# Kernel tuning notes

Hardware: AMD Instinct MI355X
Metric: run time of the kernel (lower is better)

## Reference

```python
import jax, jax.numpy as jnp
import numpy as np

EPS = 1e-5
MOM = 0.9

def _ln(x, g, b):
    m = jnp.mean(x, axis=-1, keepdims=True)
    v = jnp.var(x, axis=-1, keepdims=True)
    return (x - m) / jnp.sqrt(v + EPS) * g + b

def _gelu(x):
    return jax.nn.gelu(x, approximate=False)  # torch default exact GELU


def setup_inputs() -> dict:
    S, B, d, K = 2048, 64, 256, 16
    key = jax.random.key(0)
    ks = jax.random.split(key, 12)
    def w(k, shape):
        return jax.random.normal(k, shape, dtype=jnp.float32) * 0.02
    return {
        'x': jax.random.normal(ks[0], (S, B, d), dtype=jnp.float32),
        'slot_init': w(ks[1], (K, d)),
        # Linear weights stored as (in, out): y = x @ W + b
        'Wq': w(ks[2], (d, d)), 'bq': jnp.zeros((d,), jnp.float32),
        'Wk': w(ks[3], (d, d)), 'bk': jnp.zeros((d,), jnp.float32),
        'Wv': w(ks[4], (d, d)), 'bv': jnp.zeros((d,), jnp.float32),
        'wg1_W': w(ks[5], (2 * d, d)), 'wg1_b': jnp.zeros((d,), jnp.float32),
        'wg2_W': w(ks[6], (d, 1)), 'wg2_b': jnp.zeros((1,), jnp.float32),
        'eg_W': w(ks[7], (2 * d, d)), 'eg_b': jnp.zeros((d,), jnp.float32),
        'wc_W': w(ks[8], (2 * d, d)), 'wc_b': jnp.zeros((d,), jnp.float32),
        'wc_ln_g': jnp.ones((d,), jnp.float32), 'wc_ln_b': jnp.zeros((d,), jnp.float32),
        'fu_W': w(ks[9], (2 * d, d)), 'fu_b': jnp.zeros((d,), jnp.float32),
        'fu_ln_g': jnp.ones((d,), jnp.float32), 'fu_ln_b': jnp.zeros((d,), jnp.float32),
        'on_g': jnp.ones((d,), jnp.float32), 'on_b': jnp.zeros((d,), jnp.float32),
    }


def reference(x, slot_init, Wq, bq, Wk, bk, Wv, bv, wg1_W, wg1_b, wg2_W, wg2_b,
              eg_W, eg_b, wc_W, wc_b, wc_ln_g, wc_ln_b, fu_W, fu_b,
              fu_ln_g, fu_ln_b, on_g, on_b):
    S, B, d = x.shape
    K = slot_init.shape[0]
    scale = d ** (-0.5)
    M0 = jnp.broadcast_to(slot_init[None], (B, K, d))            # [B,K,d]
    p0 = jnp.zeros((B, K), x.dtype)

    def step(carry, x_t):
        M, pers = carry
        q = x_t @ Wq + bq                                        # [B,d]
        k = M @ Wk + bk                                          # [B,K,d]
        v = M @ Wv + bv
        attn = jax.nn.softmax(jnp.einsum('bd,bkd->bk', q, k) * scale, axis=-1)
        r = jnp.einsum('bk,bkd->bd', attn, v)                    # [B,d]
        pers = MOM * pers + (1.0 - MOM) * attn
        cat = jnp.concatenate([x_t, r], axis=-1)                 # [B,2d]
        out_t = _ln(_gelu(cat @ fu_W + fu_b), fu_ln_g, fu_ln_b)  # dropout = eval/identity
        novelty = 1.0 - jnp.max(attn, axis=-1, keepdims=True)    # [B,1]
        g_w = jax.nn.sigmoid(_gelu(cat @ wg1_W + wg1_b) @ wg2_W + wg2_b) * novelty
        evict = jax.nn.softmax(-pers * 4.0, axis=-1)             # [B,K]
        sq = jnp.concatenate([jnp.broadcast_to(x_t[:, None], (B, K, d)), M], axis=-1)
        erase = jax.nn.sigmoid(sq @ eg_W + eg_b)                 # [B,K,d]
        write = _ln(_gelu(sq @ wc_W + wc_b), wc_ln_g, wc_ln_b)
        alpha = (g_w * evict)[..., None]                         # [B,K,1]
        M = M * (1.0 - alpha * erase) + alpha * write
        pers = pers + evict * g_w * 0.1
        return (M, pers), out_t

    (M, _), outs = jax.lax.scan(step, (M0, p0), x)
    x_aug = _ln(outs + x, on_g, on_b)                            # [S,B,d]
    proto = jnp.transpose(M, (1, 0, 2))                          # [K,B,d]
    return x_aug, proto
```

## Files before the change

### kernel.cpp

```cpp
#include <hip/hip_runtime.h>
#include <stdint.h>
#include <stddef.h>


#define SLEN 2048
#define NB   64
#define DD   256
#define KS   16
#define KVSTR 1026
#define TPB  512

typedef __attribute__((ext_vector_type(8))) short v8bf;
typedef __attribute__((ext_vector_type(4))) float v4f;

__device__ __forceinline__ float bf2f(uint16_t h){
  union { uint32_t u; float f; } v; v.u = ((uint32_t)h) << 16; return v.f;
}
__device__ __forceinline__ uint16_t f2bf(float f){
  union { float f; uint32_t u; } v; v.f = f;
  uint32_t u = v.u;
  return (uint16_t)((u + 0x7FFFu + ((u >> 16) & 1u)) >> 16);
}
__device__ __forceinline__ void splitf(float f, uint16_t& h, uint16_t& l){
  h = f2bf(f);
  l = f2bf(f - bf2f(h));
}
__device__ __forceinline__ float geluf(float xx){
  return 0.5f * xx * (1.0f + erff(xx * 0.70710678118654752f));
}
__device__ __forceinline__ float sigmf(float xx){
  return 1.0f / (1.0f + expf(-xx));
}
__device__ __forceinline__ v4f MFMA16(v8bf a, v8bf b, v4f c){
  return __builtin_amdgcn_mfma_f32_16x16x32_bf16(a, b, c, 0, 0, 0);
}

template<int RM>
__device__ __forceinline__ void ldA_f32(const char* base, int lane, int kc,
                                        v8bf& hi, v8bf& lo){
  int row = lane & RM;
  int off = row * 1024 + (((kc << 7) + ((lane >> 4) << 5)) ^ ((row & 7) << 5));
  const float* p = (const float*)(base + off);
  union { v8bf v; uint16_t u[8]; } H, L;
  #pragma unroll
  for (int j = 0; j < 8; ++j) splitf(p[j], H.u[j], L.u[j]);
  hi = H.v; lo = L.v;
}

__global__ __launch_bounds__(256) void prep_kernel(
    const float* __restrict__ Wq, const float* __restrict__ Wk, const float* __restrict__ Wv,
    const float* __restrict__ wg1W, const float* __restrict__ egW, const float* __restrict__ wcW,
    const float* __restrict__ fuW,
    const float* __restrict__ bq, const float* __restrict__ bwg1, const float* __restrict__ beg,
    const float* __restrict__ bwc, const float* __restrict__ bfu,
    const float* __restrict__ bk, const float* __restrict__ bv,
    uint16_t* __restrict__ wbigh, uint16_t* __restrict__ wbigl,
    uint16_t* __restrict__ wrfh,
    uint16_t* __restrict__ wxfh, uint16_t* __restrict__ wxfl,
    float* __restrict__ bxall, float* __restrict__ bkv)
{
  int idx = blockIdx.x * 256 + threadIdx.x;
  if (idx < 262144){
    int j = idx & 7, lane = (idx >> 3) & 63, kc = (idx >> 9) & 7, nt = idx >> 12;
    int k = kc*32 + ((lane >> 4) << 3) + j;
    int n = nt*16 + (lane & 15);
    float v;
    if (n < 256)      v = Wk[k*256 + n];
    else if (n < 512) v = Wv[k*256 + n - 256];
    else if (n < 768) v = egW[(256 + k)*256 + n - 512];
    else              v = wcW[(256 + k)*256 + n - 768];
    uint16_t h, l; splitf(v, h, l);
    wbigh[idx] = h; wbigl[idx] = l;
  }
  int i2 = idx - 262144;
  if (i2 >= 0 && i2 < 131072){
    int j = i2 & 7, lane = (i2 >> 3) & 63, kc = (i2 >> 9) & 7, nt = i2 >> 12;
    int k = kc*32 + ((lane >> 4) << 3) + j;
    int n = nt*16 + (lane & 15);
    float v = (n < 256) ? wg1W[(256 + k)*256 + n] : fuW[(256 + k)*256 + n - 256];
    wrfh[i2] = f2bf(v);
  }
  int i3 = idx - 393216;
  if (i3 >= 0 && i3 < 327680){
    int j = i3 & 7, lane = (i3 >> 3) & 63, kc = (i3 >> 9) & 7, nt = i3 >> 12;
    int k = kc*32 + ((lane >> 4) << 3) + j;
    int n = nt*16 + (lane & 15);
    float v;
    if (n < 256)       v = Wq[k*256 + n];
    else if (n < 512)  v = wg1W[k*256 + n - 256];
    else if (n < 768)  v = egW[k*256 + n - 512];
    else if (n < 1024) v = wcW[k*256 + n - 768];
    else               v = fuW[k*256 + n - 1024];
    uint16_t h, l; splitf(v, h, l);
    wxfh[i3] = h; wxfl[i3] = l;
  }
  int i4 = idx - 720896;
  if (i4 >= 0 && i4 < 1280){
    float v;
    if (i4 < 256)       v = bq[i4];
    else if (i4 < 512)  v = bwg1[i4 - 256];
    else if (i4 < 768)  v = beg[i4 - 512];
    else if (i4 < 1024) v = bwc[i4 - 768];
    else                v = bfu[i4 - 1024];
    bxall[i4] = v;
  }
  int i5 = idx - 722176;
  if (i5 >= 0 && i5 < 512){
    bkv[i5] = (i5 < 256) ? bk[i5] : bv[i5 - 256];
  }
}

#define SM_BYTES 134544

__global__ __launch_bounds__(TPB, 2) void memunit_kernel(
    const float* __restrict__ x, const float* __restrict__ slot_init,
    const float* __restrict__ wg2W, const float* __restrict__ wg2b,
    const float* __restrict__ wcg, const float* __restrict__ wcb,
    const float* __restrict__ fug, const float* __restrict__ fub,
    const float* __restrict__ ong, const float* __restrict__ onb,
    const uint16_t* __restrict__ wbigh, const uint16_t* __restrict__ wbigl,
    const uint16_t* __restrict__ wrfh,
    const uint16_t* __restrict__ wxfh, const uint16_t* __restrict__ wxfl,
    const float* __restrict__ bxall, const float* __restrict__ bkv,
    float* __restrict__ out)
{
  extern __shared__ char smem[];
  char*     MfB  = smem;
  char*     xbB  = smem + 16384;
  char*     rbB  = smem + 24576;
  float*    rb   = (float*)rbB;
  float*    kveg = (float*)(smem + 25600);
  float*    Xp   = (float*)(smem + 91264);
  float*    mv   = (float*)(smem + 132224);
  float*    sc   = (float*)(smem + 134272);

  const int b    = blockIdx.x;
  const int tid  = threadIdx.x;
  const int lane = tid & 63;
  const int wave = tid >> 6;
  const int grp  = tid & 31;

  const float wg2b0 = wg2b[0];

  auto mfp = [&](int s, int n) -> float* {
    return (float*)(MfB + s*1024 + (((n*4)) ^ ((s & 7) << 5)));
  };

  {
    int s = tid >> 5;
    int c0 = grp * 8;
    #pragma unroll
    for (int jj = 0; jj < 8; ++jj)
      *mfp(s, c0 + jj) = slot_init[s*256 + c0 + jj];
    if (tid < 256) rb[tid] = 0.0f;
    if (tid < 16)  sc[16 + tid] = 0.0f;
  }
  __syncthreads();

  for (int t = 0; t < SLEN; ++t){
    const int tt = t & 7;

    auto update_row = [&](int s, float gw_){
      float wp[8]; float s1 = 0.f, s2 = 0.f;
      #pragma unroll
      for (int jj = 0; jj < 8; ++jj){
        int n = grp + jj*32;
        float wv = geluf(kveg[s*KVSTR + 768 + n] + Xp[tt*1280 + 768 + n]);
        wp[jj] = wv; s1 += wv; s2 += wv*wv;
      }
      #pragma unroll
      for (int mm = 16; mm >= 1; mm >>= 1){
        s1 += __shfl_xor(s1, mm); s2 += __shfl_xor(s2, mm);
      }
      float mean = s1 * (1.0f/256.0f);
      float rs = 1.0f / sqrtf(s2 * (1.0f/256.0f) - mean*mean + 1e-5f);
      float al = gw_ * sc[32 + s];
      #pragma unroll
      for (int jj = 0; jj < 8; ++jj){
        int n = grp + jj*32;
        float er = sigmf(kveg[s*KVSTR + 512 + n] + Xp[tt*1280 + 512 + n]);
        float wn = (wp[jj] - mean)*rs*wcg[n] + wcb[n];
        float* mp = mfp(s, n);
        float m0 = *mp;
        *mp = m0*(1.0f - al*er) + al*wn;
      }
    };

    if (tt == 0){
      {
        int row = tid >> 6;
        int c0 = (tid & 63) * 4;
        v4f xv4 = *(const v4f*)(x + ((size_t)(t + row) * NB + b) * DD + c0);
        *(v4f*)(xbB + row*1024 + ((c0*4) ^ ((row & 7) << 5))) = xv4;
      }
      __syncthreads();
      {
        v8bf axh[8], axl[8];
        #pragma unroll
        for (int kc = 0; kc < 8; ++kc) ldA_f32<7>(xbB, lane, kc, axh[kc], axl[kc]);
        #pragma unroll
        for (int i = 0; i < 10; ++i){
          int nt = wave * 10 + i;
          const v8bf* bph = ((const v8bf*)wxfh) + (nt*8)*64 + lane;
          const v8bf* bpl = ((const v8bf*)wxfl) + (nt*8)*64 + lane;
          v8bf bh[8], bl[8];
          #pragma unroll
          for (int kc = 0; kc < 8; ++kc){ bh[kc] = bph[kc*64]; bl[kc] = bpl[kc*64]; }
          v4f acc = {0.f, 0.f, 0.f, 0.f};
          #pragma unroll
          for (int kc = 0; kc < 8; ++kc) acc = MFMA16(axh[kc], bh[kc], acc);
          #pragma unroll
          for (int kc = 0; kc < 8; ++kc) acc = MFMA16(axh[kc], bl[kc], acc);
          #pragma unroll
          for (int kc = 0; kc < 8; ++kc) acc = MFMA16(axl[kc], bh[kc], acc);
          int r0 = (lane >> 4) << 2;
          if (r0 < 8){
            int n = nt*16 + (lane & 15);
            float bias = bxall[n];
            #pragma unroll
            for (int r = 0; r < 4; ++r) Xp[(r0 + r)*1280 + n] = acc[r] + bias;
          }
        }
      }
      __syncthreads();
    }

    {
      v8bf amh[8], aml[8];
      #pragma unroll
      for (int kc = 0; kc < 8; ++kc) ldA_f32<15>(MfB, lane, kc, amh[kc], aml[kc]);
      #pragma unroll
      for (int i = 0; i < 8; ++i){
        int nt = wave * 8 + i;
        const v8bf* bph = ((const v8bf*)wbigh) + (nt*8)*64 + lane;
        const v8bf* bpl = ((const v8bf*)wbigl) + (nt*8)*64 + lane;
        v8bf bh[8], bl[8];
        #pragma unroll
        for (int kc = 0; kc < 8; ++kc){ bh[kc] = bph[kc*64]; bl[kc] = bpl[kc*64]; }
        v4f acc = {0.f, 0.f, 0.f, 0.f};
        #pragma unroll
        for (int kc = 0; kc < 8; ++kc) acc = MFMA16(amh[kc], bh[kc], acc);
        #pragma unroll
        for (int kc = 0; kc < 8; ++kc) acc = MFMA16(amh[kc], bl[kc], acc);
        #pragma unroll
        for (int kc = 0; kc < 8; ++kc) acc = MFMA16(aml[kc], bh[kc], acc);
        int n = nt*16 + (lane & 15);
        float bias = (n < 512) ? bkv[n] : 0.0f;
        int r0 = (lane >> 4) << 2;
        #pragma unroll
        for (int r = 0; r < 4; ++r) kveg[(r0 + r)*KVSTR + n] = acc[r] + bias;
      }
    }
    __syncthreads();

    {
      int s = tid >> 5;
      float p = 0.f;
      #pragma unroll
      for (int it = 0; it < 8; ++it){
        int j = grp + it*32;
        p += Xp[tt*1280 + j] * kveg[s*KVSTR + j];
      }
      #pragma unroll
      for (int mm = 16; mm >= 1; mm >>= 1) p += __shfl_xor(p, mm);
      if (grp == 0) sc[s] = p * 0.0625f;
    }
    __syncthreads();

    float nov;
    {
      float lg[16];
      float mx = -1e30f;
      #pragma unroll
      for (int s2 = 0; s2 < 16; ++s2){ lg[s2] = sc[s2]; mx = fmaxf(mx, lg[s2]); }
      float at[16]; float ssum = 0.f;
      #pragma unroll
      for (int s2 = 0; s2 < 16; ++s2){ at[s2] = expf(lg[s2] - mx); ssum += at[s2]; }
      float inv = 1.0f / ssum;
      nov = 1.0f - inv;
      if (tid < 256){
        float rv = 0.f;
        #pragma unroll
        for (int s2 = 0; s2 < 16; ++s2) rv += (at[s2] * inv) * kveg[s2*KVSTR + 256 + tid];
        rb[tid] = rv;
      }
      if (tid < 16) sc[16 + tid] = 0.9f*sc[16 + tid] + 0.1f*(at[tid]*inv);
    }
    __syncthreads();

    if (tid < 16){
      float pv[16]; float mx = -1e30f;
      #pragma unroll
      for (int i = 0; i < 16; ++i){ pv[i] = -4.0f * sc[16 + i]; mx = fmaxf(mx, pv[i]); }
      float ev[16]; float ssum = 0.f;
      #pragma unroll
      for (int i = 0; i < 16; ++i){ ev[i] = expf(pv[i] - mx); ssum += ev[i]; }
      sc[32 + tid] = ev[tid] / ssum;
    }
    {
      v8bf arh[8], arl[8];
      #pragma unroll
      for (int kc = 0; kc < 8; ++kc) ldA_f32<0>(rbB, lane, kc, arh[kc], arl[kc]);
      #pragma unroll
      for (int i = 0; i < 4; ++i){
        int nt = wave*4 + i;
        const v8bf* bph = ((const v8bf*)wrfh) + (nt*8)*64 + lane;
        v8bf bh[8];
        #pragma unroll
        for (int kc = 0; kc < 8; ++kc) bh[kc] = bph[kc*64];
        v4f acc = {0.f, 0.f, 0.f, 0.f};
        #pragma unroll
        for (int kc = 0; kc < 8; ++kc) acc = MFMA16(arh[kc], bh[kc], acc);
        #pragma unroll
        for (int kc = 0; kc < 8; ++kc) acc = MFMA16(arl[kc], bh[kc], acc);
        if (lane < 16) mv[nt*16 + lane] = acc[0];
      }
    }
    __syncthreads();

    float fpre = 0.f;
    if (tid < 256){
      float gp = geluf(Xp[tt*1280 + 256 + tid] + mv[tid]) * wg2W[tid];
      #pragma unroll
      for (int mm = 32; mm >= 1; mm >>= 1) gp += __shfl_xor(gp, mm);
      if (lane == 0) sc[48 + wave] = gp;
    } else {
      int j = tid - 256;
      fpre = geluf(Xp[tt*1280 + 1024 + j] + mv[256 + j]);
      float s1 = fpre, s2 = fpre*fpre;
      #pragma unroll
      for (int mm = 32; mm >= 1; mm >>= 1){ s1 += __shfl_xor(s1, mm); s2 += __shfl_xor(s2, mm); }
      if (lane == 0){ sc[52 + 2*(wave-4)] = s1; sc[52 + 2*(wave-4) + 1] = s2; }
    }
    __syncthreads();

    const float gw = sigmf(sc[48] + sc[49] + sc[50] + sc[51] + wg2b0) * nov;

    float y = 0.f;
    if (tid < 256){
      update_row(tid >> 5, gw);
      if (tid < 16) sc[16 + tid] += sc[32 + tid] * gw * 0.1f;
    } else {
      int j = tid - 256;
      float fm = (sc[52] + sc[54] + sc[56] + sc[58]) * (1.0f/256.0f);
      float fq = (sc[53] + sc[55] + sc[57] + sc[59]) * (1.0f/256.0f);
      float o = (fpre - fm) * (1.0f / sqrtf(fq - fm*fm + 1e-5f)) * fug[j] + fub[j];
      float xv = *(const float*)(xbB + tt*1024 + ((j*4) ^ ((tt & 7) << 5)));
      y = o + xv;
      float s1 = y, s2 = y*y;
      #pragma unroll
      for (int mm = 32; mm >= 1; mm >>= 1){ s1 += __shfl_xor(s1, mm); s2 += __shfl_xor(s2, mm); }
      if (lane == 0){ sc[60 + 2*(wave-4)] = s1; sc[60 + 2*(wave-4) + 1] = s2; }
    }
    __syncthreads();

    if (tid >= 256){
      int j = tid - 256;
      float m2 = (sc[60] + sc[62] + sc[64] + sc[66]) * (1.0f/256.0f);
      float q2 = (sc[61] + sc[63] + sc[65] + sc[67]) * (1.0f/256.0f);
      out[(size_t)t*NB*DD + (size_t)b*DD + j] =
          (y - m2) * (1.0f / sqrtf(q2 - m2*m2 + 1e-5f)) * ong[j] + onb[j];
      update_row(8 + ((tid - 256) >> 5), gw);
    }
    __syncthreads();
  }

  {
    int s = tid >> 5;
    size_t base = (size_t)SLEN*NB*DD + ((size_t)s*NB + b)*DD;
    #pragma unroll
    for (int jj = 0; jj < 8; ++jj){
      int n = grp + jj*32;
      out[base + n] = *mfp(s, n);
    }
  }
}

extern "C" void kernel_launch(void* const* d_in, const int* in_sizes, int n_in,
                              void* d_out, int out_size, void* d_ws, size_t ws_size,
                              hipStream_t stream)
{
  const float* x     = (const float*)d_in[0];
  const float* si    = (const float*)d_in[1];
  const float* Wq    = (const float*)d_in[2];
  const float* bq    = (const float*)d_in[3];
  const float* Wk    = (const float*)d_in[4];
  const float* bk    = (const float*)d_in[5];
  const float* Wv    = (const float*)d_in[6];
  const float* bv    = (const float*)d_in[7];
  const float* wg1W  = (const float*)d_in[8];
  const float* wg1b  = (const float*)d_in[9];
  const float* wg2W  = (const float*)d_in[10];
  const float* wg2b  = (const float*)d_in[11];
  const float* egW   = (const float*)d_in[12];
  const float* egb   = (const float*)d_in[13];
  const float* wcW   = (const float*)d_in[14];
  const float* wcb   = (const float*)d_in[15];
  const float* wclng = (const float*)d_in[16];
  const float* wclnb = (const float*)d_in[17];
  const float* fuW   = (const float*)d_in[18];
  const float* fub   = (const float*)d_in[19];
  const float* fulng = (const float*)d_in[20];
  const float* fulnb = (const float*)d_in[21];
  const float* ong   = (const float*)d_in[22];
  const float* onb   = (const float*)d_in[23];
  float* out = (float*)d_out;

  char* ws = (char*)d_ws;
  uint16_t* wbigh = (uint16_t*)(ws);
  uint16_t* wbigl = (uint16_t*)(ws + 524288);
  uint16_t* wrfh  = (uint16_t*)(ws + 1048576);
  uint16_t* wxfh  = (uint16_t*)(ws + 1310720);
  uint16_t* wxfl  = (uint16_t*)(ws + 1966080);
  float* bxall    = (float*)(ws + 2621440);
  float* bkv      = (float*)(ws + 2626560);

  hipLaunchKernelGGL(prep_kernel, dim3(2823), dim3(256), 0, stream,
                     Wq, Wk, Wv, wg1W, egW, wcW, fuW,
                     bq, wg1b, egb, wcb, fub, bk, bv,
                     wbigh, wbigl, wrfh, wxfh, wxfl, bxall, bkv);

  hipFuncSetAttribute(reinterpret_cast<const void*>(memunit_kernel),
                      hipFuncAttributeMaxDynamicSharedMemorySize, SM_BYTES);
  hipLaunchKernelGGL(memunit_kernel, dim3(NB), dim3(TPB), SM_BYTES, stream,
                     x, si, wg2W, wg2b, wclng, wclnb, fulng, fulnb, ong, onb,
                     wbigh, wbigl, wrfh, wxfh, wxfl, bxall, bkv, out);
}
```

Measured before the change: 141.7 ms.

## Pack two batch rows per block and precompute x projections in a separate kernel

Each 512-thread block now handles two batch elements with 256 threads each, so the grid drops from 64 to 32 blocks. The per-step M projections are split into two phases, with the erase and write matmul overlapped after the r computation. A new xproj_kernel precomputes the x-side projections for all timesteps into workspace when it is large enough, taking that matmul off the sequential recurrence. The cost is fewer waves per batch element, more sequential MFMA work per wave, and a large global buffer read back each step group.

```diff
diff --git a/kernel.cpp b/kernel.cpp
--- a/kernel.cpp
+++ b/kernel.cpp
@@ -6,9 +6,8 @@
 #define SLEN 2048
 #define NB   64
 #define DD   256
-#define KS   16
-#define KVSTR 1026
 #define TPB  512
+#define KVS  520
 
 typedef __attribute__((ext_vector_type(8))) short v8bf;
 typedef __attribute__((ext_vector_type(4))) float v4f;
@@ -110,7 +109,55 @@
   }
 }
 
-#define SM_BYTES 134544
+__global__ __launch_bounds__(256) void xproj_kernel(
+    const float* __restrict__ x,
+    const uint16_t* __restrict__ wxfh, const uint16_t* __restrict__ wxfl,
+    const float* __restrict__ bxall, float* __restrict__ Xpg)
+{
+  __shared__ char xs[16384];
+  const int tid = threadIdx.x;
+  const int lane = tid & 63;
+  const int wv = tid >> 6;
+  const int r0 = blockIdx.x * 16;
+  {
+    int row = tid >> 4;
+    int c0 = (tid & 15) * 16;
+    const float* xp = x + (size_t)(r0 + row) * 256 + c0;
+    #pragma unroll
+    for (int q = 0; q < 4; ++q){
+      v4f v = *(const v4f*)(xp + q*4);
+      int c = c0 + q*4;
+      *(v4f*)(xs + row*1024 + ((c*4) ^ ((row & 7) << 5))) = v;
+    }
+  }
+  __syncthreads();
+  v8bf ah[8], al[8];
+  #pragma unroll
+  for (int kc = 0; kc < 8; ++kc) ldA_f32<15>(xs, lane, kc, ah[kc], al[kc]);
+  for (int i = 0; i < 20; ++i){
+    int nt = wv * 20 + i;
+    const v8bf* bph = ((const v8bf*)wxfh) + (nt*8)*64 + lane;
+    const v8bf* bpl = ((const v8bf*)wxfl) + (nt*8)*64 + lane;
+    v8bf bh[8], bl[8];
+    #pragma unroll
+    for (int kc = 0; kc < 8; ++kc){ bh[kc] = bph[kc*64]; bl[kc] = bpl[kc*64]; }
+    v4f acc = {0.f, 0.f, 0.f, 0.f};
+    #pragma unroll
+    for (int kc = 0; kc < 8; ++kc) acc = MFMA16(ah[kc], bh[kc], acc);
+    #pragma unroll
+    for (int kc = 0; kc < 8; ++kc) acc = MFMA16(ah[kc], bl[kc], acc);
+    #pragma unroll
+    for (int kc = 0; kc < 8; ++kc) acc = MFMA16(al[kc], bh[kc], acc);
+    int n = nt*16 + (lane & 15);
+    int rr = (lane >> 4) * 4;
+    float bias = bxall[n];
+    #pragma unroll
+    for (int r = 0; r < 4; ++r)
+      Xpg[(size_t)(r0 + rr + r) * 1280 + n] = acc[r] + bias;
+  }
+}
+
+#define SM_BYTES 155648
 
 __global__ __launch_bounds__(TPB, 2) void memunit_kernel(
     const float* __restrict__ x, const float* __restrict__ slot_init,
@@ -122,85 +169,70 @@
     const uint16_t* __restrict__ wrfh,
     const uint16_t* __restrict__ wxfh, const uint16_t* __restrict__ wxfl,
     const float* __restrict__ bxall, const float* __restrict__ bkv,
+    const float* __restrict__ Xpg, int use_pre,
     float* __restrict__ out)
 {
   extern __shared__ char smem[];
-  char*     MfB  = smem;
-  char*     xbB  = smem + 16384;
-  char*     rbB  = smem + 24576;
-  float*    rb   = (float*)rbB;
-  float*    kveg = (float*)(smem + 25600);
-  float*    Xp   = (float*)(smem + 91264);
-  float*    mv   = (float*)(smem + 132224);
-  float*    sc   = (float*)(smem + 134272);
-
-  const int b    = blockIdx.x;
   const int tid  = threadIdx.x;
   const int lane = tid & 63;
   const int wave = tid >> 6;
-  const int grp  = tid & 31;
+  const int bi   = tid >> 8;
+  const int bt   = tid & 255;
+  const int gwv  = wave & 3;
+  const int gb   = blockIdx.x * 2 + bi;
+
+  char*  MfB = smem + bi*16384;
+  char*  xbB = smem + 32768 + bi*4096;
+  float* xp  = (float*)(smem + 40960) + bi*(4*1280);
+  float* kv  = (float*)(smem + 81920) + bi*(16*KVS);
+  char*  rbB = smem + 148480 + bi*1024;
+  float* rb  = (float*)rbB;
+  float* mvB = (float*)(smem + 150528) + bi*512;
+  float* scB = (float*)(smem + 154624) + bi*128;
 
   const float wg2b0 = wg2b[0];
 
   auto mfp = [&](int s, int n) -> float* {
-    return (float*)(MfB + s*1024 + (((n*4)) ^ ((s & 7) << 5)));
+    return (float*)(MfB + s*1024 + ((n*4) ^ ((s & 7) << 5)));
   };
 
   {
-    int s = tid >> 5;
-    int c0 = grp * 8;
-    #pragma unroll
-    for (int jj = 0; jj < 8; ++jj)
+    int s = bt >> 4;
+    int c0 = (bt & 15) * 16;
+    #pragma unroll
+    for (int jj = 0; jj < 16; ++jj)
       *mfp(s, c0 + jj) = slot_init[s*256 + c0 + jj];
-    if (tid < 256) rb[tid] = 0.0f;
-    if (tid < 16)  sc[16 + tid] = 0.0f;
+    rb[bt & 255 & 0xFF] = 0.0f;
+    rb[bt] = 0.0f;
+    if (bt < 68) scB[bt] = 0.0f;
   }
   __syncthreads();
 
   for (int t = 0; t < SLEN; ++t){
-    const int tt = t & 7;
-
-    auto update_row = [&](int s, float gw_){
-      float wp[8]; float s1 = 0.f, s2 = 0.f;
-      #pragma unroll
-      for (int jj = 0; jj < 8; ++jj){
-        int n = grp + jj*32;
-        float wv = geluf(kveg[s*KVSTR + 768 + n] + Xp[tt*1280 + 768 + n]);
-        wp[jj] = wv; s1 += wv; s2 += wv*wv;
-      }
-      #pragma unroll
-      for (int mm = 16; mm >= 1; mm >>= 1){
-        s1 += __shfl_xor(s1, mm); s2 += __shfl_xor(s2, mm);
-      }
-      float mean = s1 * (1.0f/256.0f);
-      float rs = 1.0f / sqrtf(s2 * (1.0f/256.0f) - mean*mean + 1e-5f);
-      float al = gw_ * sc[32 + s];
-      #pragma unroll
-      for (int jj = 0; jj < 8; ++jj){
-        int n = grp + jj*32;
-        float er = sigmf(kveg[s*KVSTR + 512 + n] + Xp[tt*1280 + 512 + n]);
-        float wn = (wp[jj] - mean)*rs*wcg[n] + wcb[n];
-        float* mp = mfp(s, n);
-        float m0 = *mp;
-        *mp = m0*(1.0f - al*er) + al*wn;
-      }
-    };
+    const int tt = t & 3;
 
     if (tt == 0){
       {
-        int row = tid >> 6;
-        int c0 = (tid & 63) * 4;
-        v4f xv4 = *(const v4f*)(x + ((size_t)(t + row) * NB + b) * DD + c0);
-        *(v4f*)(xbB + row*1024 + ((c0*4) ^ ((row & 7) << 5))) = xv4;
-      }
-      __syncthreads();
-      {
-        v8bf axh[8], axl[8];
-        #pragma unroll
-        for (int kc = 0; kc < 8; ++kc) ldA_f32<7>(xbB, lane, kc, axh[kc], axl[kc]);
-        #pragma unroll
-        for (int i = 0; i < 10; ++i){
-          int nt = wave * 10 + i;
+        int row = bt >> 6;
+        int c0 = (bt & 63) * 4;
+        v4f xv4 = *(const v4f*)(x + ((size_t)(t + row) * NB + gb) * DD + c0);
+        *(v4f*)(xbB + row*1024 + ((c0*4) ^ (row << 5))) = xv4;
+      }
+      if (use_pre){
+        #pragma unroll
+        for (int w = 0; w < 4; ++w){
+          const float* src = Xpg + ((size_t)(t + w) * NB + gb) * 1280;
+          #pragma unroll
+          for (int kq = 0; kq < 5; ++kq)
+            xp[w*1280 + bt + kq*256] = src[bt + kq*256];
+        }
+      } else {
+        __syncthreads();
+        v8bf ah[8], al[8];
+        #pragma unroll
+        for (int kc = 0; kc < 8; ++kc) ldA_f32<3>(xbB, lane, kc, ah[kc], al[kc]);
+        for (int i = 0; i < 20; ++i){
+          int nt = gwv * 20 + i;
           const v8bf* bph = ((const v8bf*)wxfh) + (nt*8)*64 + lane;
           const v8bf* bpl = ((const v8bf*)wxfl) + (nt*8)*64 + lane;
           v8bf bh[8], bl[8];
@@ -208,30 +240,27 @@
           for (int kc = 0; kc < 8; ++kc){ bh[kc] = bph[kc*64]; bl[kc] = bpl[kc*64]; }
           v4f acc = {0.f, 0.f, 0.f, 0.f};
           #pragma unroll
-          for (int kc = 0; kc < 8; ++kc) acc = MFMA16(axh[kc], bh[kc], acc);
+          for (int kc = 0; kc < 8; ++kc) acc = MFMA16(ah[kc], bh[kc], acc);
           #pragma unroll
-          for (int kc = 0; kc < 8; ++kc) acc = MFMA16(axh[kc], bl[kc], acc);
+          for (int kc = 0; kc < 8; ++kc) acc = MFMA16(ah[kc], bl[kc], acc);
           #pragma unroll
-          for (int kc = 0; kc < 8; ++kc) acc = MFMA16(axl[kc], bh[kc], acc);
-          int r0 = (lane >> 4) << 2;
-          if (r0 < 8){
+          for (int kc = 0; kc < 8; ++kc) acc = MFMA16(al[kc], bh[kc], acc);
+          if ((lane >> 4) == 0){
             int n = nt*16 + (lane & 15);
             float bias = bxall[n];
             #pragma unroll
-            for (int r = 0; r < 4; ++r) Xp[(r0 + r)*1280 + n] = acc[r] + bias;
+            for (int r = 0; r < 4; ++r) xp[r*1280 + n] = acc[r] + bias;
           }
         }
       }
-      __syncthreads();
     }
 
     {
       v8bf amh[8], aml[8];
       #pragma unroll
       for (int kc = 0; kc < 8; ++kc) ldA_f32<15>(MfB, lane, kc, amh[kc], aml[kc]);
-      #pragma unroll
       for (int i = 0; i < 8; ++i){
-        int nt = wave * 8 + i;
+        int nt = gwv * 8 + i;
         const v8bf* bph = ((const v8bf*)wbigh) + (nt*8)*64 + lane;
         const v8bf* bpl = ((const v8bf*)wbigl) + (nt*8)*64 + lane;
         v8bf bh[8], bl[8];
@@ -245,65 +274,61 @@
         #pragma unroll
         for (int kc = 0; kc < 8; ++kc) acc = MFMA16(aml[kc], bh[kc], acc);
         int n = nt*16 + (lane & 15);
-        float bias = (n < 512) ? bkv[n] : 0.0f;
-        int r0 = (lane >> 4) << 2;
-        #pragma unroll
-        for (int r = 0; r < 4; ++r) kveg[(r0 + r)*KVSTR + n] = acc[r] + bias;
-      }
-    }
-    __syncthreads();
-
-    {
-      int s = tid >> 5;
+        float bias = bkv[n];
+        int r0 = (lane >> 4) * 4;
+        #pragma unroll
+        for (int r = 0; r < 4; ++r) kv[(r0 + r)*KVS + n] = acc[r] + bias;
+      }
+    }
+    __syncthreads();
+
+    {
+      int s = bt >> 4;
       float p = 0.f;
       #pragma unroll
-      for (int it = 0; it < 8; ++it){
-        int j = grp + it*32;
-        p += Xp[tt*1280 + j] * kveg[s*KVSTR + j];
-      }
-      #pragma unroll
-      for (int mm = 16; mm >= 1; mm >>= 1) p += __shfl_xor(p, mm);
-      if (grp == 0) sc[s] = p * 0.0625f;
+      for (int it = 0; it < 16; ++it){
+        int j = (bt & 15) + it*16;
+        p += xp[tt*1280 + j] * kv[s*KVS + j];
+      }
+      #pragma unroll
+      for (int mm = 8; mm >= 1; mm >>= 1) p += __shfl_xor(p, mm);
+      if ((bt & 15) == 0) scB[s] = p * 0.0625f;
     }
     __syncthreads();
 
     float nov;
     {
-      float lg[16];
-      float mx = -1e30f;
-      #pragma unroll
-      for (int s2 = 0; s2 < 16; ++s2){ lg[s2] = sc[s2]; mx = fmaxf(mx, lg[s2]); }
+      float lg[16]; float mx = -1e30f;
+      #pragma unroll
+      for (int s2 = 0; s2 < 16; ++s2){ lg[s2] = scB[s2]; mx = fmaxf(mx, lg[s2]); }
       float at[16]; float ssum = 0.f;
       #pragma unroll
       for (int s2 = 0; s2 < 16; ++s2){ at[s2] = expf(lg[s2] - mx); ssum += at[s2]; }
       float inv = 1.0f / ssum;
       nov = 1.0f - inv;
-      if (tid < 256){
-        float rv = 0.f;
-        #pragma unroll
-        for (int s2 = 0; s2 < 16; ++s2) rv += (at[s2] * inv) * kveg[s2*KVSTR + 256 + tid];
-        rb[tid] = rv;
-      }
-      if (tid < 16) sc[16 + tid] = 0.9f*sc[16 + tid] + 0.1f*(at[tid]*inv);
-    }
-    __syncthreads();
-
-    if (tid < 16){
+      float rv = 0.f;
+      #pragma unroll
+      for (int s2 = 0; s2 < 16; ++s2) rv += (at[s2] * inv) * kv[s2*KVS + 256 + bt];
+      rb[bt] = rv;
+      if (bt < 16) scB[16 + bt] = 0.9f*scB[16 + bt] + 0.1f*(at[bt]*inv);
+    }
+    __syncthreads();
+
+    if (bt < 16){
       float pv[16]; float mx = -1e30f;
       #pragma unroll
-      for (int i = 0; i < 16; ++i){ pv[i] = -4.0f * sc[16 + i]; mx = fmaxf(mx, pv[i]); }
+      for (int i = 0; i < 16; ++i){ pv[i] = -4.0f * scB[16 + i]; mx = fmaxf(mx, pv[i]); }
       float ev[16]; float ssum = 0.f;
       #pragma unroll
       for (int i = 0; i < 16; ++i){ ev[i] = expf(pv[i] - mx); ssum += ev[i]; }
-      sc[32 + tid] = ev[tid] / ssum;
+      scB[32 + bt] = ev[bt] / ssum;
     }
     {
       v8bf arh[8], arl[8];
       #pragma unroll
       for (int kc = 0; kc < 8; ++kc) ldA_f32<0>(rbB, lane, kc, arh[kc], arl[kc]);
-      #pragma unroll
-      for (int i = 0; i < 4; ++i){
-        int nt = wave*4 + i;
+      for (int i = 0; i < 8; ++i){
+        int nt = gwv * 8 + i;
         const v8bf* bph = ((const v8bf*)wrfh) + (nt*8)*64 + lane;
         v8bf bh[8];
         #pragma unroll
@@ -313,64 +338,108 @@
         for (int kc = 0; kc < 8; ++kc) acc = MFMA16(arh[kc], bh[kc], acc);
         #pragma unroll
         for (int kc = 0; kc < 8; ++kc) acc = MFMA16(arl[kc], bh[kc], acc);
-        if (lane < 16) mv[nt*16 + lane] = acc[0];
-      }
-    }
-    __syncthreads();
-
-    float fpre = 0.f;
-    if (tid < 256){
-      float gp = geluf(Xp[tt*1280 + 256 + tid] + mv[tid]) * wg2W[tid];
-      #pragma unroll
-      for (int mm = 32; mm >= 1; mm >>= 1) gp += __shfl_xor(gp, mm);
-      if (lane == 0) sc[48 + wave] = gp;
-    } else {
-      int j = tid - 256;
-      fpre = geluf(Xp[tt*1280 + 1024 + j] + mv[256 + j]);
+        if (lane < 16) mvB[nt*16 + lane] = acc[0];
+      }
+    }
+    {
+      v8bf amh[8], aml[8];
+      #pragma unroll
+      for (int kc = 0; kc < 8; ++kc) ldA_f32<15>(MfB, lane, kc, amh[kc], aml[kc]);
+      for (int i = 0; i < 8; ++i){
+        int nt = 32 + gwv * 8 + i;
+        const v8bf* bph = ((const v8bf*)wbigh) + (nt*8)*64 + lane;
+        const v8bf* bpl = ((const v8bf*)wbigl) + (nt*8)*64 + lane;
+        v8bf bh[8], bl[8];
+        #pragma unroll
+        for (int kc = 0; kc < 8; ++kc){ bh[kc] = bph[kc*64]; bl[kc] = bpl[kc*64]; }
+        v4f acc = {0.f, 0.f, 0.f, 0.f};
+        #pragma unroll
+        for (int kc = 0; kc < 8; ++kc) acc = MFMA16(amh[kc], bh[kc], acc);
+        #pragma unroll
+        for (int kc = 0; kc < 8; ++kc) acc = MFMA16(amh[kc], bl[kc], acc);
+        #pragma unroll
+        for (int kc = 0; kc < 8; ++kc) acc = MFMA16(aml[kc], bh[kc], acc);
+        int n = (nt - 32)*16 + (lane & 15);
+        int r0 = (lane >> 4) * 4;
+        #pragma unroll
+        for (int r = 0; r < 4; ++r) kv[(r0 + r)*KVS + n] = acc[r];
+      }
+    }
+    __syncthreads();
+
+    float gp = geluf(xp[tt*1280 + 256 + bt] + mvB[bt]) * wg2W[bt];
+    float fpre = geluf(xp[tt*1280 + 1024 + bt] + mvB[256 + bt]);
+    {
       float s1 = fpre, s2 = fpre*fpre;
       #pragma unroll
-      for (int mm = 32; mm >= 1; mm >>= 1){ s1 += __shfl_xor(s1, mm); s2 += __shfl_xor(s2, mm); }
-      if (lane == 0){ sc[52 + 2*(wave-4)] = s1; sc[52 + 2*(wave-4) + 1] = s2; }
-    }
-    __syncthreads();
-
-    const float gw = sigmf(sc[48] + sc[49] + sc[50] + sc[51] + wg2b0) * nov;
-
-    float y = 0.f;
-    if (tid < 256){
-      update_row(tid >> 5, gw);
-      if (tid < 16) sc[16 + tid] += sc[32 + tid] * gw * 0.1f;
-    } else {
-      int j = tid - 256;
-      float fm = (sc[52] + sc[54] + sc[56] + sc[58]) * (1.0f/256.0f);
-      float fq = (sc[53] + sc[55] + sc[57] + sc[59]) * (1.0f/256.0f);
-      float o = (fpre - fm) * (1.0f / sqrtf(fq - fm*fm + 1e-5f)) * fug[j] + fub[j];
-      float xv = *(const float*)(xbB + tt*1024 + ((j*4) ^ ((tt & 7) << 5)));
+      for (int mm = 32; mm >= 1; mm >>= 1){
+        gp += __shfl_xor(gp, mm);
+        s1 += __shfl_xor(s1, mm); s2 += __shfl_xor(s2, mm);
+      }
+      if (lane == 0){
+        scB[48 + gwv] = gp;
+        scB[52 + 2*gwv] = s1; scB[53 + 2*gwv] = s2;
+      }
+    }
+    __syncthreads();
+
+    const float gw = sigmf(scB[48] + scB[49] + scB[50] + scB[51] + wg2b0) * nov;
+    float y;
+    {
+      float fm = (scB[52] + scB[54] + scB[56] + scB[58]) * (1.0f/256.0f);
+      float fq = (scB[53] + scB[55] + scB[57] + scB[59]) * (1.0f/256.0f);
+      float o = (fpre - fm) * (1.0f / sqrtf(fq - fm*fm + 1e-5f)) * fug[bt] + fub[bt];
+      float xv = *(const float*)(xbB + tt*1024 + ((bt*4) ^ (tt << 5)));
       y = o + xv;
       float s1 = y, s2 = y*y;
       #pragma unroll
       for (int mm = 32; mm >= 1; mm >>= 1){ s1 += __shfl_xor(s1, mm); s2 += __shfl_xor(s2, mm); }
-      if (lane == 0){ sc[60 + 2*(wave-4)] = s1; sc[60 + 2*(wave-4) + 1] = s2; }
-    }
-    __syncthreads();
-
-    if (tid >= 256){
-      int j = tid - 256;
-      float m2 = (sc[60] + sc[62] + sc[64] + sc[66]) * (1.0f/256.0f);
-      float q2 = (sc[61] + sc[63] + sc[65] + sc[67]) * (1.0f/256.0f);
-      out[(size_t)t*NB*DD + (size_t)b*DD + j] =
-          (y - m2) * (1.0f / sqrtf(q2 - m2*m2 + 1e-5f)) * ong[j] + onb[j];
-      update_row(8 + ((tid - 256) >> 5), gw);
+      if (lane == 0){ scB[60 + 2*gwv] = s1; scB[61 + 2*gwv] = s2; }
+      if (bt < 16) scB[16 + bt] += scB[32 + bt] * gw * 0.1f;
+    }
+    __syncthreads();
+
+    {
+      float m2 = (scB[60] + scB[62] + scB[64] + scB[66]) * (1.0f/256.0f);
+      float q2 = (scB[61] + scB[63] + scB[65] + scB[67]) * (1.0f/256.0f);
+      out[(size_t)t*NB*DD + (size_t)gb*DD + bt] =
+          (y - m2) * (1.0f / sqrtf(q2 - m2*m2 + 1e-5f)) * ong[bt] + onb[bt];
+
+      int s = bt >> 4;
+      int l16 = bt & 15;
+      float wp[16]; float s1 = 0.f, s2 = 0.f;
+      #pragma unroll
+      for (int jj = 0; jj < 16; ++jj){
+        int n = l16 + jj*16;
+        float wv = geluf(kv[s*KVS + 256 + n] + xp[tt*1280 + 768 + n]);
+        wp[jj] = wv; s1 += wv; s2 += wv*wv;
+      }
+      #pragma unroll
+      for (int mm = 8; mm >= 1; mm >>= 1){
+        s1 += __shfl_xor(s1, mm); s2 += __shfl_xor(s2, mm);
+      }
+      float mean = s1 * (1.0f/256.0f);
+      float rs = 1.0f / sqrtf(s2 * (1.0f/256.0f) - mean*mean + 1e-5f);
+      float al = gw * scB[32 + s];
+      #pragma unroll
+      for (int jj = 0; jj < 16; ++jj){
+        int n = l16 + jj*16;
+        float er = sigmf(kv[s*KVS + n] + xp[tt*1280 + 512 + n]);
+        float wn = (wp[jj] - mean)*rs*wcg[n] + wcb[n];
+        float* mp = mfp(s, n);
+        float m0 = *mp;
+        *mp = m0*(1.0f - al*er) + al*wn;
+      }
     }
     __syncthreads();
   }
 
   {
-    int s = tid >> 5;
-    size_t base = (size_t)SLEN*NB*DD + ((size_t)s*NB + b)*DD;
-    #pragma unroll
-    for (int jj = 0; jj < 8; ++jj){
-      int n = grp + jj*32;
+    int s = bt >> 4;
+    size_t base = (size_t)SLEN*NB*DD + ((size_t)s*NB + gb)*DD;
+    #pragma unroll
+    for (int jj = 0; jj < 16; ++jj){
+      int n = (bt & 15) + jj*16;
       out[base + n] = *mfp(s, n);
     }
   }
@@ -414,15 +483,25 @@
   uint16_t* wxfl  = (uint16_t*)(ws + 1966080);
   float* bxall    = (float*)(ws + 2621440);
   float* bkv      = (float*)(ws + 2626560);
+  const size_t xpg_off = 2631680;
+  float* Xpg      = (float*)(ws + xpg_off);
+  const size_t need = xpg_off + (size_t)SLEN * NB * 1280 * 4;
+  const int use_pre = (ws_size >= need) ? 1 : 0;
 
   hipLaunchKernelGGL(prep_kernel, dim3(2823), dim3(256), 0, stream,
                      Wq, Wk, Wv, wg1W, egW, wcW, fuW,
                      bq, wg1b, egb, wcb, fub, bk, bv,
                      wbigh, wbigl, wrfh, wxfh, wxfl, bxall, bkv);
 
+  if (use_pre){
+    hipLaunchKernelGGL(xproj_kernel, dim3(SLEN*NB/16), dim3(256), 0, stream,
+                       x, wxfh, wxfl, bxall, Xpg);
+  }
+
   hipFuncSetAttribute(reinterpret_cast<const void*>(memunit_kernel),
                       hipFuncAttributeMaxDynamicSharedMemorySize, SM_BYTES);
-  hipLaunchKernelGGL(memunit_kernel, dim3(NB), dim3(TPB), SM_BYTES, stream,
+  hipLaunchKernelGGL(memunit_kernel, dim3(NB/2), dim3(TPB), SM_BYTES, stream,
                      x, si, wg2W, wg2b, wclng, wclnb, fulng, fulnb, ong, onb,
-                     wbigh, wbigl, wrfh, wxfh, wxfl, bxall, bkv, out);
-}
+                     wbigh, wbigl, wrfh, wxfh, wxfl, bxall, bkv,
+                     Xpg, use_pre, out);
+}
```

Measured after the change: 227.6 ms. 60.7% more time.

## Precompute x projections in separate kernel, pipeline weight loads, cache wrf in registers

Applied to the files above, without the earlier changes.

Moves the per-timestep x-dependent projections (q, wg1, eg, wc, fu input halves) out of the sequential scan into a fully parallel xproj_kernel that writes them to a large workspace buffer. The scan kernel then copies those values instead of running MFMAs every eighth step. The kv/eg/wc GEMM weight loads are software-pipelined with triple buffering, the fu/wg1 r-weights are held in registers for the whole scan, and the kv stride is padded. The precompute path depends on workspace size, and the extra registers needed force launch bounds down to one block per CU.

```diff
diff --git a/kernel.cpp b/kernel.cpp
--- a/kernel.cpp
+++ b/kernel.cpp
@@ -6,9 +6,8 @@
 #define SLEN 2048
 #define NB   64
 #define DD   256
-#define KS   16
-#define KVSTR 1026
 #define TPB  512
+#define KVSTR 1028
 
 typedef __attribute__((ext_vector_type(8))) short v8bf;
 typedef __attribute__((ext_vector_type(4))) float v4f;
@@ -110,9 +109,72 @@
   }
 }
 
-#define SM_BYTES 134544
-
-__global__ __launch_bounds__(TPB, 2) void memunit_kernel(
+__global__ __launch_bounds__(256) void xproj_kernel(
+    const float* __restrict__ x,
+    const uint16_t* __restrict__ wxfh, const uint16_t* __restrict__ wxfl,
+    const float* __restrict__ bxall, float* __restrict__ Xpg)
+{
+  __shared__ char xs[16384];
+  const int tid = threadIdx.x;
+  const int lane = tid & 63;
+  const int wv = tid >> 6;
+  const int r0 = blockIdx.x * 16;
+  {
+    int row = tid >> 4;
+    int c0 = (tid & 15) * 16;
+    const float* xp = x + (size_t)(r0 + row) * 256 + c0;
+    #pragma unroll
+    for (int q = 0; q < 4; ++q){
+      v4f v = *(const v4f*)(xp + q*4);
+      int c = c0 + q*4;
+      *(v4f*)(xs + row*1024 + ((c*4) ^ ((row & 7) << 5))) = v;
+    }
+  }
+  __syncthreads();
+  v8bf ah[8], al[8];
+  #pragma unroll
+  for (int kc = 0; kc < 8; ++kc) ldA_f32<15>(xs, lane, kc, ah[kc], al[kc]);
+  for (int i = 0; i < 20; ++i){
+    int nt = wv * 20 + i;
+    const v8bf* bph = ((const v8bf*)wxfh) + (nt*8)*64 + lane;
+    const v8bf* bpl = ((const v8bf*)wxfl) + (nt*8)*64 + lane;
+    v8bf bh[8], bl[8];
+    #pragma unroll
+    for (int kc = 0; kc < 8; ++kc){ bh[kc] = bph[kc*64]; bl[kc] = bpl[kc*64]; }
+    v4f acc = {0.f, 0.f, 0.f, 0.f};
+    #pragma unroll
+    for (int kc = 0; kc < 8; ++kc) acc = MFMA16(ah[kc], bh[kc], acc);
+    #pragma unroll
+    for (int kc = 0; kc < 8; ++kc) acc = MFMA16(ah[kc], bl[kc], acc);
+    #pragma unroll
+    for (int kc = 0; kc < 8; ++kc) acc = MFMA16(al[kc], bh[kc], acc);
+    int n = nt*16 + (lane & 15);
+    int rr = (lane >> 4) * 4;
+    float bias = bxall[n];
+    #pragma unroll
+    for (int r = 0; r < 4; ++r)
+      Xpg[(size_t)(r0 + rr + r) * 1280 + n] = acc[r] + bias;
+  }
+}
+
+#define SM_BYTES 134672
+
+#define G1_ISSUE(H, L, ii) \
+  { const int off_ = ((wave*8 + (ii))*8)*64 + lane; \
+    _Pragma("unroll") for (int kc = 0; kc < 8; ++kc){ \
+      H[kc] = pbh_[off_ + kc*64]; L[kc] = pbl_[off_ + kc*64]; } }
+
+#define G1_CONS(H, L, ii) \
+  { v4f acc_ = {0.f,0.f,0.f,0.f}; \
+    _Pragma("unroll") for (int kc = 0; kc < 8; ++kc) acc_ = MFMA16(amh[kc], H[kc], acc_); \
+    _Pragma("unroll") for (int kc = 0; kc < 8; ++kc) acc_ = MFMA16(amh[kc], L[kc], acc_); \
+    _Pragma("unroll") for (int kc = 0; kc < 8; ++kc) acc_ = MFMA16(aml[kc], H[kc], acc_); \
+    const int n_ = (wave*8 + (ii))*16 + (lane & 15); \
+    const float bias_ = (wave < 4) ? bkvR[(ii)] : 0.0f; \
+    const int r0_ = (lane >> 4) << 2; \
+    _Pragma("unroll") for (int r = 0; r < 4; ++r) kv[(r0_ + r)*KVSTR + n_] = acc_[r] + bias_; }
+
+__global__ __launch_bounds__(TPB, 1) void memunit_kernel(
     const float* __restrict__ x, const float* __restrict__ slot_init,
     const float* __restrict__ wg2W, const float* __restrict__ wg2b,
     const float* __restrict__ wcg, const float* __restrict__ wcb,
@@ -122,17 +184,18 @@
     const uint16_t* __restrict__ wrfh,
     const uint16_t* __restrict__ wxfh, const uint16_t* __restrict__ wxfl,
     const float* __restrict__ bxall, const float* __restrict__ bkv,
+    const float* __restrict__ Xpg, int use_pre,
     float* __restrict__ out)
 {
   extern __shared__ char smem[];
-  char*     MfB  = smem;
-  char*     xbB  = smem + 16384;
-  char*     rbB  = smem + 24576;
-  float*    rb   = (float*)rbB;
-  float*    kveg = (float*)(smem + 25600);
-  float*    Xp   = (float*)(smem + 91264);
-  float*    mv   = (float*)(smem + 132224);
-  float*    sc   = (float*)(smem + 134272);
+  char*  MfB = smem;
+  char*  xbB = smem + 16384;
+  char*  rbB = smem + 24576;
+  float* rb  = (float*)rbB;
+  float* kv  = (float*)(smem + 25600);
+  float* Xp  = (float*)(smem + 91392);
+  float* mv  = (float*)(smem + 132352);
+  float* sc  = (float*)(smem + 134400);
 
   const int b    = blockIdx.x;
   const int tid  = threadIdx.x;
@@ -141,10 +204,26 @@
   const int grp  = tid & 31;
 
   const float wg2b0 = wg2b[0];
+  const v8bf* __restrict__ pbh_ = (const v8bf*)wbigh;
+  const v8bf* __restrict__ pbl_ = (const v8bf*)wbigl;
 
   auto mfp = [&](int s, int n) -> float* {
-    return (float*)(MfB + s*1024 + (((n*4)) ^ ((s & 7) << 5)));
+    return (float*)(MfB + s*1024 + ((n*4) ^ ((s & 7) << 5)));
   };
+
+  v8bf wr[32];
+  {
+    const v8bf* wp = ((const v8bf*)wrfh) + lane;
+    #pragma unroll
+    for (int i = 0; i < 4; ++i)
+      #pragma unroll
+      for (int kc = 0; kc < 8; ++kc)
+        wr[i*8 + kc] = wp[((wave*4 + i)*8 + kc)*64];
+  }
+  float bkvR[8];
+  #pragma unroll
+  for (int i = 0; i < 8; ++i)
+    bkvR[i] = (wave < 4) ? bkv[(wave*8 + i)*16 + (lane & 15)] : 0.0f;
 
   {
     int s = tid >> 5;
@@ -165,7 +244,7 @@
       #pragma unroll
       for (int jj = 0; jj < 8; ++jj){
         int n = grp + jj*32;
-        float wv = geluf(kveg[s*KVSTR + 768 + n] + Xp[tt*1280 + 768 + n]);
+        float wv = geluf(kv[s*KVSTR + 768 + n] + Xp[tt*1280 + 768 + n]);
         wp[jj] = wv; s1 += wv; s2 += wv*wv;
       }
       #pragma unroll
@@ -178,7 +257,7 @@
       #pragma unroll
       for (int jj = 0; jj < 8; ++jj){
         int n = grp + jj*32;
-        float er = sigmf(kveg[s*KVSTR + 512 + n] + Xp[tt*1280 + 512 + n]);
+        float er = sigmf(kv[s*KVSTR + 512 + n] + Xp[tt*1280 + 512 + n]);
         float wn = (wp[jj] - mean)*rs*wcg[n] + wcb[n];
         float* mp = mfp(s, n);
         float m0 = *mp;
@@ -193,12 +272,21 @@
         v4f xv4 = *(const v4f*)(x + ((size_t)(t + row) * NB + b) * DD + c0);
         *(v4f*)(xbB + row*1024 + ((c0*4) ^ ((row & 7) << 5))) = xv4;
       }
-      __syncthreads();
-      {
-        v8bf axh[8], axl[8];
+      if (use_pre){
+        int row = tid >> 6;
+        int l6 = tid & 63;
+        const float* src = Xpg + ((size_t)(t + row) * NB + b) * 1280;
+        float* dst = Xp + row*1280;
         #pragma unroll
-        for (int kc = 0; kc < 8; ++kc) ldA_f32<7>(xbB, lane, kc, axh[kc], axl[kc]);
+        for (int q = 0; q < 5; ++q){
+          int c = (l6 + 64*q) * 4;
+          *(v4f*)(dst + c) = *(const v4f*)(src + c);
+        }
+      } else {
+        __syncthreads();
+        v8bf ah[8], al8[8];
         #pragma unroll
+        for (int kc = 0; kc < 8; ++kc) ldA_f32<7>(xbB, lane, kc, ah[kc], al8[kc]);
         for (int i = 0; i < 10; ++i){
           int nt = wave * 10 + i;
           const v8bf* bph = ((const v8bf*)wxfh) + (nt*8)*64 + lane;
@@ -208,11 +296,11 @@
           for (int kc = 0; kc < 8; ++kc){ bh[kc] = bph[kc*64]; bl[kc] = bpl[kc*64]; }
           v4f acc = {0.f, 0.f, 0.f, 0.f};
           #pragma unroll
-          for (int kc = 0; kc < 8; ++kc) acc = MFMA16(axh[kc], bh[kc], acc);
+          for (int kc = 0; kc < 8; ++kc) acc = MFMA16(ah[kc], bh[kc], acc);
           #pragma unroll
-          for (int kc = 0; kc < 8; ++kc) acc = MFMA16(axh[kc], bl[kc], acc);
+          for (int kc = 0; kc < 8; ++kc) acc = MFMA16(ah[kc], bl[kc], acc);
           #pragma unroll
-          for (int kc = 0; kc < 8; ++kc) acc = MFMA16(axl[kc], bh[kc], acc);
+          for (int kc = 0; kc < 8; ++kc) acc = MFMA16(al8[kc], bh[kc], acc);
           int r0 = (lane >> 4) << 2;
           if (r0 < 8){
             int n = nt*16 + (lane & 15);
@@ -222,34 +310,24 @@
           }
         }
       }
-      __syncthreads();
     }
 
     {
+      v8bf h0[8], l0[8], h1[8], l1[8], h2[8], l2[8];
+      G1_ISSUE(h0, l0, 0)
+      G1_ISSUE(h1, l1, 1)
+      G1_ISSUE(h2, l2, 2)
       v8bf amh[8], aml[8];
       #pragma unroll
       for (int kc = 0; kc < 8; ++kc) ldA_f32<15>(MfB, lane, kc, amh[kc], aml[kc]);
-      #pragma unroll
-      for (int i = 0; i < 8; ++i){
-        int nt = wave * 8 + i;
-        const v8bf* bph = ((const v8bf*)wbigh) + (nt*8)*64 + lane;
-        const v8bf* bpl = ((const v8bf*)wbigl) + (nt*8)*64 + lane;
-        v8bf bh[8], bl[8];
-        #pragma unroll
-        for (int kc = 0; kc < 8; ++kc){ bh[kc] = bph[kc*64]; bl[kc] = bpl[kc*64]; }
-        v4f acc = {0.f, 0.f, 0.f, 0.f};
-        #pragma unroll
-        for (int kc = 0; kc < 8; ++kc) acc = MFMA16(amh[kc], bh[kc], acc);
-        #pragma unroll
-        for (int kc = 0; kc < 8; ++kc) acc = MFMA16(amh[kc], bl[kc], acc);
-        #pragma unroll
-        for (int kc = 0; kc < 8; ++kc) acc = MFMA16(aml[kc], bh[kc], acc);
-        int n = nt*16 + (lane & 15);
-        float bias = (n < 512) ? bkv[n] : 0.0f;
-        int r0 = (lane >> 4) << 2;
-        #pragma unroll
-        for (int r = 0; r < 4; ++r) kveg[(r0 + r)*KVSTR + n] = acc[r] + bias;
-      }
+      G1_CONS(h0, l0, 0)  G1_ISSUE(h0, l0, 3)
+      G1_CONS(h1, l1, 1)  G1_ISSUE(h1, l1, 4)
+      G1_CONS(h2, l2, 2)  G1_ISSUE(h2, l2, 5)
+      G1_CONS(h0, l0, 3)  G1_ISSUE(h0, l0, 6)
+      G1_CONS(h1, l1, 4)  G1_ISSUE(h1, l1, 7)
+      G1_CONS(h2, l2, 5)
+      G1_CONS(h0, l0, 6)
+      G1_CONS(h1, l1, 7)
     }
     __syncthreads();
 
@@ -259,7 +337,7 @@
       #pragma unroll
       for (int it = 0; it < 8; ++it){
         int j = grp + it*32;
-        p += Xp[tt*1280 + j] * kveg[s*KVSTR + j];
+        p += Xp[tt*1280 + j] * kv[s*KVSTR + j];
       }
       #pragma unroll
       for (int mm = 16; mm >= 1; mm >>= 1) p += __shfl_xor(p, mm);
@@ -269,8 +347,7 @@
 
     float nov;
     {
-      float lg[16];
-      float mx = -1e30f;
+      float lg[16]; float mx = -1e30f;
       #pragma unroll
       for (int s2 = 0; s2 < 16; ++s2){ lg[s2] = sc[s2]; mx = fmaxf(mx, lg[s2]); }
       float at[16]; float ssum = 0.f;
@@ -281,7 +358,7 @@
       if (tid < 256){
         float rv = 0.f;
         #pragma unroll
-        for (int s2 = 0; s2 < 16; ++s2) rv += (at[s2] * inv) * kveg[s2*KVSTR + 256 + tid];
+        for (int s2 = 0; s2 < 16; ++s2) rv += (at[s2] * inv) * kv[s2*KVSTR + 256 + tid];
         rb[tid] = rv;
       }
       if (tid < 16) sc[16 + tid] = 0.9f*sc[16 + tid] + 0.1f*(at[tid]*inv);
@@ -303,17 +380,12 @@
       for (int kc = 0; kc < 8; ++kc) ldA_f32<0>(rbB, lane, kc, arh[kc], arl[kc]);
       #pragma unroll
       for (int i = 0; i < 4; ++i){
-        int nt = wave*4 + i;
-        const v8bf* bph = ((const v8bf*)wrfh) + (nt*8)*64 + lane;
-        v8bf bh[8];
-        #pragma unroll
-        for (int kc = 0; kc < 8; ++kc) bh[kc] = bph[kc*64];
         v4f acc = {0.f, 0.f, 0.f, 0.f};
         #pragma unroll
-        for (int kc = 0; kc < 8; ++kc) acc = MFMA16(arh[kc], bh[kc], acc);
+        for (int kc = 0; kc < 8; ++kc) acc = MFMA16(arh[kc], wr[i*8 + kc], acc);
         #pragma unroll
-        for (int kc = 0; kc < 8; ++kc) acc = MFMA16(arl[kc], bh[kc], acc);
-        if (lane < 16) mv[nt*16 + lane] = acc[0];
+        for (int kc = 0; kc < 8; ++kc) acc = MFMA16(arl[kc], wr[i*8 + kc], acc);
+        if (lane < 16) mv[(wave*4 + i)*16 + lane] = acc[0];
       }
     }
     __syncthreads();
@@ -414,15 +486,25 @@
   uint16_t* wxfl  = (uint16_t*)(ws + 1966080);
   float* bxall    = (float*)(ws + 2621440);
   float* bkv      = (float*)(ws + 2626560);
+  const size_t xpg_off = 2631680;
+  float* Xpg      = (float*)(ws + xpg_off);
+  const size_t need = xpg_off + (size_t)SLEN * NB * 1280 * 4;
+  const int use_pre = (ws_size >= need) ? 1 : 0;
 
   hipLaunchKernelGGL(prep_kernel, dim3(2823), dim3(256), 0, stream,
                      Wq, Wk, Wv, wg1W, egW, wcW, fuW,
                      bq, wg1b, egb, wcb, fub, bk, bv,
                      wbigh, wbigl, wrfh, wxfh, wxfl, bxall, bkv);
 
+  if (use_pre){
+    hipLaunchKernelGGL(xproj_kernel, dim3(SLEN*NB/16), dim3(256), 0, stream,
+                       x, wxfh, wxfl, bxall, Xpg);
+  }
+
   hipFuncSetAttribute(reinterpret_cast<const void*>(memunit_kernel),
                       hipFuncAttributeMaxDynamicSharedMemorySize, SM_BYTES);
   hipLaunchKernelGGL(memunit_kernel, dim3(NB), dim3(TPB), SM_BYTES, stream,
                      x, si, wg2W, wg2b, wclng, wclnb, fulng, fulnb, ong, onb,
-                     wbigh, wbigl, wrfh, wxfh, wxfl, bxall, bkv, out);
-}
+                     wbigh, wbigl, wrfh, wxfh, wxfl, bxall, bkv,
+                     Xpg, use_pre, out);
+}
```

Measured after the change: 141.1 ms. No clear change (-0.4%).
